# Kernel tuning notes

Measured on AMD Instinct MI355X. Metric: run time of the kernel, lower is better.

The kernel has to match this reference:

```python
import jax, jax.numpy as jnp
import numpy as np

H = 32          # num_attention_heads
KVH = 8         # num_key_value_heads
D = 2048        # hidden_size
HD = D // H     # attention_head_size = 64
REP = H // KVH  # queries per kv head = 4


def setup_inputs() -> dict:
    key = jax.random.key(0)
    ks = jax.random.split(key, 7)
    s = 0.02
    return {
        "hidden_states": jax.random.normal(ks[0], (2, 2048, D), dtype=jnp.float32),
        "Wq": jax.random.normal(ks[1], (D, D), dtype=jnp.float32) * s,
        "bq": jax.random.normal(ks[2], (D,), dtype=jnp.float32) * s,
        "Wk": jax.random.normal(ks[3], (D, KVH * HD), dtype=jnp.float32) * s,
        "bk": jax.random.normal(ks[4], (KVH * HD,), dtype=jnp.float32) * s,
        "Wv": jax.random.normal(ks[5], (D, KVH * HD), dtype=jnp.float32) * s,
        "bv": jax.random.normal(ks[6], (KVH * HD,), dtype=jnp.float32) * s,
    }


def _split_heads(x, n_heads):
    # [B, S, n_heads*HD] -> [B, n_heads, S, HD]
    b, s, _ = x.shape
    return x.reshape(b, s, n_heads, HD).transpose(0, 2, 1, 3)


def reference(hidden_states, Wq, bq, Wk, bk, Wv, bv):
    b, s, _ = hidden_states.shape
    q = _split_heads(hidden_states @ Wq + bq, H)          # [B,H,S,HD]
    k = _split_heads(hidden_states @ Wk + bk, KVH)        # [B,KVH,S,HD]
    v = _split_heads(hidden_states @ Wv + bv, KVH)
    # repeat KV heads to match query heads (q_idx // REP -> kv_idx)
    k = jnp.repeat(k, REP, axis=1)                         # [B,H,S,HD]
    v = jnp.repeat(v, REP, axis=1)
    scores = jnp.einsum("bhqd,bhkd->bhqk", q, k) / jnp.sqrt(jnp.float32(HD))
    probs = jax.nn.softmax(scores, axis=-1)
    ctx = jnp.einsum("bhqk,bhkd->bhqd", probs, v)          # [B,H,S,HD]
    ctx = ctx.transpose(0, 2, 1, 3).reshape(b, s, H * HD)
    return ctx
```

## Files before the change

### kernel.cpp

```cpp
#include <hip/hip_runtime.h>
#include <hip/hip_bf16.h>

#define NH 32
#define NKVH 8
#define DMODEL 2048
#define HDIM 64
#define NB 2
#define SEQ 2048
#define MROWS (NB*SEQ)
#define NQ 2048
#define NKV 512
#define NTOT 3072
#define NT (SEQ/64)

typedef __bf16 bf16x4 __attribute__((ext_vector_type(4)));
typedef __bf16 bf16x8 __attribute__((ext_vector_type(8)));
typedef float  f32x2  __attribute__((ext_vector_type(2)));
typedef float  f32x4  __attribute__((ext_vector_type(4)));
typedef float  f32x16 __attribute__((ext_vector_type(16)));
typedef unsigned u32x2 __attribute__((ext_vector_type(2)));
typedef unsigned u32x4 __attribute__((ext_vector_type(4)));

__device__ inline __bf16 f2bf(float f) {
    unsigned u = __builtin_bit_cast(unsigned, f);
    u += 0x7fff + ((u >> 16) & 1);
    unsigned short s = (unsigned short)(u >> 16);
    return __builtin_bit_cast(__bf16, s);
}

__device__ inline unsigned pack2bf(float a, float b) {
    unsigned ua = __builtin_bit_cast(unsigned, a);
    ua += 0x7fff + ((ua >> 16) & 1);
    unsigned ub = __builtin_bit_cast(unsigned, b);
    ub += 0x7fff + ((ub >> 16) & 1);
    return (ua >> 16) | (ub & 0xffff0000u);
}

__device__ inline void gload_lds16(const void* g, void* l) {
    __builtin_amdgcn_global_load_lds(
        (const __attribute__((address_space(1))) void*)g,
        (__attribute__((address_space(3))) void*)l, 16, 0, 0);
}

__device__ inline float max3f(float a, float b, float c) {
    float r;
    asm("v_max3_f32 %0, %1, %2, %3" : "=v"(r) : "v"(a), "v"(b), "v"(c));
    return r;
}

__device__ inline float cross_max32(float x) {
#if __has_builtin(__builtin_amdgcn_permlane32_swap)
    unsigned xu = __builtin_bit_cast(unsigned, x);
    u32x2 r = __builtin_amdgcn_permlane32_swap(xu, xu, false, false);
    return fmaxf(__builtin_bit_cast(float, r[0]), __builtin_bit_cast(float, r[1]));
#else
    return fmaxf(x, __shfl_xor(x, 32));
#endif
}

__global__ __launch_bounds__(256)
void cvt_hs(const float* __restrict__ Hs, __bf16* __restrict__ Ab)
{
    size_t idx = ((size_t)blockIdx.x * 256 + threadIdx.x) * 8;
    f32x4 a = *reinterpret_cast<const f32x4*>(Hs + idx);
    f32x4 b = *reinterpret_cast<const f32x4*>(Hs + idx + 4);
    u32x4 w;
    w[0] = pack2bf(a[0], a[1]); w[1] = pack2bf(a[2], a[3]);
    w[2] = pack2bf(b[0], b[1]); w[3] = pack2bf(b[2], b[3]);
    *reinterpret_cast<u32x4*>((char*)Ab + idx * 2) = w;
}

__global__ __launch_bounds__(256)
void transpose_w(const float* __restrict__ Wq,
                 const float* __restrict__ Wk,
                 const float* __restrict__ Wv,
                 __bf16* __restrict__ Wt)
{
    __shared__ __bf16 tile[64][72];
    int k0 = blockIdx.x * 64;
    int n0 = blockIdx.y * 64;
    const float* Wsrc; int ncols; int nbase;
    if (n0 < NQ)            { Wsrc = Wq; ncols = NQ;  nbase = n0; }
    else if (n0 < NQ + NKV) { Wsrc = Wk; ncols = NKV; nbase = n0 - NQ; }
    else                    { Wsrc = Wv; ncols = NKV; nbase = n0 - NQ - NKV; }
    int t = threadIdx.x;
    int kl = t >> 2;
    int nc = (t & 3) * 16;
    const float* src = Wsrc + (size_t)(k0 + kl) * ncols + nbase + nc;
    #pragma unroll
    for (int i = 0; i < 4; ++i) {
        f32x4 v = *reinterpret_cast<const f32x4*>(src + i * 4);
        #pragma unroll
        for (int e = 0; e < 4; ++e) tile[kl][nc + i * 4 + e] = f2bf(v[e]);
    }
    __syncthreads();
    int nl = t >> 2;
    int kc = (t & 3) * 16;
    bf16x8 o0, o1;
    #pragma unroll
    for (int i = 0; i < 8; ++i) o0[i] = tile[kc + i][nl];
    #pragma unroll
    for (int i = 0; i < 8; ++i) o1[i] = tile[kc + 8 + i][nl];
    __bf16* dst = Wt + (size_t)(n0 + nl) * DMODEL + k0 + kc;
    *reinterpret_cast<bf16x8*>(dst)     = o0;
    *reinterpret_cast<bf16x8*>(dst + 8) = o1;
}

#define BM 128
#define BN 128
#define BK 64

__global__ __launch_bounds__(256)
void qkv_gemm(const __bf16* __restrict__ Ab,
              const __bf16* __restrict__ Wt,
              const float* __restrict__ bq,
              const float* __restrict__ bk,
              const float* __restrict__ bv,
              __bf16* __restrict__ Qb,
              __bf16* __restrict__ Kb,
              __bf16* __restrict__ Vt)
{
    __shared__ char lds[32768];

    int bid = blockIdx.x;
    int xcd = bid & 7, r = bid >> 3;
    int rm = r / 12, rn = r % 12;
    int m0 = ((xcd >> 1) * 8 + rm) * BM;
    int n0 = ((xcd & 1) * 12 + rn) * BN;

    int t = threadIdx.x;
    int wave = t >> 6, lane = t & 63;
    int g = lane >> 4, lh = lane & 15;
    int wr = wave >> 1, wc = wave & 1;

    int srow = wave * 8 + (lane >> 3);
    int schunk = (lane & 7) ^ (lane >> 3);
    const char* Asrc = (const char*)Ab + (size_t)(m0 + srow) * 4096 + schunk * 16;
    const char* Bsrc = (const char*)Wt + (size_t)(n0 + srow) * 4096 + schunk * 16;
    int dstw = wave * 1024;

    f32x4 acc[4][4] = {};

    for (int k0 = 0; k0 < DMODEL * 2; k0 += BK * 2) {
        #pragma unroll
        for (int i = 0; i < 4; ++i)
            gload_lds16(Asrc + (size_t)i * 32 * 4096 + k0, lds + i * 4096 + dstw);
        #pragma unroll
        for (int i = 0; i < 4; ++i)
            gload_lds16(Bsrc + (size_t)i * 32 * 4096 + k0, lds + 16384 + i * 4096 + dstw);
        __syncthreads();
        #pragma unroll
        for (int kk = 0; kk < 2; ++kk) {
            bf16x8 af[4], bfr[4];
            #pragma unroll
            for (int mi = 0; mi < 4; ++mi) {
                int row = wr * 64 + mi * 16 + lh;
                int byte = row * 128 + (((kk * 4 + g) ^ (lh & 7)) << 4);
                af[mi] = *reinterpret_cast<const bf16x8*>(lds + byte);
            }
            #pragma unroll
            for (int ni = 0; ni < 4; ++ni) {
                int row = wc * 64 + ni * 16 + lh;
                int byte = row * 128 + (((kk * 4 + g) ^ (lh & 7)) << 4);
                bfr[ni] = *reinterpret_cast<const bf16x8*>(lds + 16384 + byte);
            }
            #pragma unroll
            for (int mi = 0; mi < 4; ++mi)
                #pragma unroll
                for (int ni = 0; ni < 4; ++ni)
                    acc[mi][ni] = __builtin_amdgcn_mfma_f32_16x16x32_bf16(af[mi], bfr[ni], acc[mi][ni], 0, 0, 0);
        }
        __syncthreads();
    }

    int mode = (n0 < NQ) ? 0 : (n0 < NQ + NKV ? 1 : 2);
    const float* bias = (mode == 0) ? bq : (mode == 1 ? bk : bv);
    int nsub = (mode == 0) ? 0 : (mode == 1 ? NQ : NQ + NKV);
    float scale = (mode == 0) ? 0.18033688011112042f : 1.0f;

    float biasv[4];
    #pragma unroll
    for (int ni = 0; ni < 4; ++ni)
        biasv[ni] = bias[n0 - nsub + wc * 64 + ni * 16 + lh];

    int gsw = ((g & 1) << 1) | (g >> 1);

    #pragma unroll
    for (int mi = 0; mi < 4; ++mi) {
        #pragma unroll
        for (int j = 0; j < 4; ++j) {
            int m = m0 + wr * 64 + mi * 16 + 4 * g + j;
            int bb = m >> 11, s = m & (SEQ - 1);
            #pragma unroll
            for (int ni = 0; ni < 4; ++ni) {
                int n = n0 + wc * 64 + ni * 16 + lh;
                __bf16 val = f2bf((acc[mi][ni][j] + biasv[ni]) * scale);
                if (mode == 0) {
                    int hh = n >> 6, d = n & 63;
                    Qb[(((size_t)bb * NH + hh) * SEQ + s) * HDIM + d] = val;
                } else if (mode == 1) {
                    int nk = n - NQ; int kv = nk >> 6, d = nk & 63;
                    Kb[(((size_t)bb * NKVH + kv) * SEQ + s) * HDIM + d] = val;
                } else {
                    int nv = n - NQ - NKV; int kv = nv >> 6, d = nv & 63;
                    int sv = (s & ~12) | (gsw << 2);
                    Vt[(((size_t)bb * NKVH + kv) * HDIM + d) * SEQ + sv] = val;
                }
            }
        }
    }
}

#define SUBSTEP(BUFB, SS) do { \
    bf16x8 kf0_ = *reinterpret_cast<const bf16x8*>(lds + (BUFB) + koff[(SS)*4 + 0]); \
    bf16x8 kf1_ = *reinterpret_cast<const bf16x8*>(lds + (BUFB) + koff[(SS)*4 + 1]); \
    bf16x8 kf2_ = *reinterpret_cast<const bf16x8*>(lds + (BUFB) + koff[(SS)*4 + 2]); \
    bf16x8 kf3_ = *reinterpret_cast<const bf16x8*>(lds + (BUFB) + koff[(SS)*4 + 3]); \
    f32x16 s_ = {}; \
    __builtin_amdgcn_s_setprio(1); \
    s_ = __builtin_amdgcn_mfma_f32_32x32x16_bf16(kf0_, qf[0], s_, 0, 0, 0); \
    s_ = __builtin_amdgcn_mfma_f32_32x32x16_bf16(kf1_, qf[1], s_, 0, 0, 0); \
    s_ = __builtin_amdgcn_mfma_f32_32x32x16_bf16(kf2_, qf[2], s_, 0, 0, 0); \
    s_ = __builtin_amdgcn_mfma_f32_32x32x16_bf16(kf3_, qf[3], s_, 0, 0, 0); \
    __builtin_amdgcn_s_setprio(0); \
    float n0_ = max3f(max3f(s_[0], s_[1], s_[2]),  max3f(s_[3], s_[4], s_[5]), \
                      max3f(s_[6], s_[7], s_[8])); \
    float n1_ = max3f(max3f(s_[9], s_[10], s_[11]), max3f(s_[12], s_[13], s_[14]), s_[15]); \
    float mt_ = cross_max32(fmaxf(n0_, n1_)); \
    if (!__all(mt_ <= m_run + 8.0f)) { \
        float mn_ = fmaxf(m_run, mt_); \
        float al_ = __builtin_amdgcn_exp2f(m_run - mn_); \
        m_run = mn_; msub = -mn_; \
        accO0 *= al_; accO1 *= al_; lsum *= al_; \
    } \
    _Pragma("unroll") \
    for (int r = 0; r < 16; ++r) s_[r] = __builtin_amdgcn_exp2f(s_[r] + msub); \
    bf16x8 pa_, pb_; \
    _Pragma("unroll") \
    for (int e = 0; e < 8; ++e) { pa_[e] = (__bf16)s_[e]; pb_[e] = (__bf16)s_[8 + e]; } \
    bf16x8 va0_ = *reinterpret_cast<const bf16x8*>(lds + (BUFB) + 8192 + koff[2 * (SS)]); \
    bf16x8 vb0_ = *reinterpret_cast<const bf16x8*>(lds + (BUFB) + 8192 + koff[2 * (SS) + 1]); \
    bf16x8 va1_ = *reinterpret_cast<const bf16x8*>(lds + (BUFB) + 8192 + koff[4 + 2 * (SS)]); \
    bf16x8 vb1_ = *reinterpret_cast<const bf16x8*>(lds + (BUFB) + 8192 + koff[4 + 2 * (SS) + 1]); \
    __builtin_amdgcn_s_setprio(1); \
    accO0 = __builtin_amdgcn_mfma_f32_32x32x16_bf16(va0_, pa_, accO0, 0, 0, 0); \
    lsum  = __builtin_amdgcn_mfma_f32_32x32x16_bf16(ones, pa_, lsum,  0, 0, 0); \
    accO0 = __builtin_amdgcn_mfma_f32_32x32x16_bf16(vb0_, pb_, accO0, 0, 0, 0); \
    lsum  = __builtin_amdgcn_mfma_f32_32x32x16_bf16(ones, pb_, lsum,  0, 0, 0); \
    accO1 = __builtin_amdgcn_mfma_f32_32x32x16_bf16(va1_, pa_, accO1, 0, 0, 0); \
    accO1 = __builtin_amdgcn_mfma_f32_32x32x16_bf16(vb1_, pb_, accO1, 0, 0, 0); \
    __builtin_amdgcn_s_setprio(0); \
} while (0)

#define TILE(BUFB, SBUFB, KT, STAGE, VM) do { \
    if (STAGE) { \
        gload_lds16(Kp + (size_t)((KT) + 2) * 8192 + kgoff, lds + (SBUFB) + kdst); \
        gload_lds16(Vp + (size_t)((KT) + 2) * 128  + vgoff, lds + (SBUFB) + vdst); \
    } \
    SUBSTEP(BUFB, 0); \
    SUBSTEP(BUFB, 1); \
    asm volatile("s_waitcnt vmcnt(" #VM ")" ::: "memory"); \
    __builtin_amdgcn_s_barrier(); \
} while (0)

__global__ __launch_bounds__(512, 4)
void attn(const __bf16* __restrict__ Qb,
          const __bf16* __restrict__ Kb,
          const __bf16* __restrict__ Vt,
          float* __restrict__ out)
{
    __shared__ char lds[65536];

    int qt = blockIdx.x;
    int bh = blockIdx.y;
    int b = bh >> 5, h = bh & 31;
    int kvh = h >> 2;
    int tid = threadIdx.x, wave = tid >> 6, lane = tid & 63;
    int ql = lane & 31, hi = lane >> 5;
    int q0 = qt * 256 + wave * 32;

    const __bf16* Qp = Qb + (size_t)(b * NH + h) * SEQ * HDIM;
    const char*   Kp = (const char*)(Kb + (size_t)(b * NKVH + kvh) * SEQ * HDIM);
    const char*   Vp = (const char*)(Vt + (size_t)(b * NKVH + kvh) * HDIM * SEQ);

    bf16x8 qf[4];
    #pragma unroll
    for (int f = 0; f < 4; ++f)
        qf[f] = *reinterpret_cast<const bf16x8*>(Qp + (size_t)(q0 + ql) * HDIM + f * 16 + hi * 8);

    u32x4 ou = { 0x3F803F80u, 0x3F803F80u, 0x3F803F80u, 0x3F803F80u };
    bf16x8 ones = __builtin_bit_cast(bf16x8, ou);

    int srow = tid >> 3;
    int schk = (tid & 7) ^ (srow & 7);
    int kgoff = srow * 128 + (schk << 4);
    size_t vgoff = (size_t)srow * (SEQ * 2) + (schk << 4);
    int kdst = tid * 16;
    int vdst = 8192 + tid * 16;

    int koff[8];
    #pragma unroll
    for (int kb = 0; kb < 2; ++kb)
        #pragma unroll
        for (int f = 0; f < 4; ++f)
            koff[kb * 4 + f] = (kb * 32 + ql) * 128 + ((f * 32 + hi * 16) ^ ((ql & 7) << 4));

    f32x16 accO0 = {}, accO1 = {}, lsum = {};
    float m_run = -1e30f, msub = 0.0f;

    gload_lds16(Kp + kgoff,        lds + kdst);
    gload_lds16(Vp + vgoff,        lds + vdst);
    gload_lds16(Kp + 8192 + kgoff, lds + 16384 + kdst);
    gload_lds16(Vp + 128  + vgoff, lds + 16384 + vdst);
    asm volatile("s_waitcnt vmcnt(2)" ::: "memory");
    __builtin_amdgcn_s_barrier();

    #pragma unroll 1
    for (int g4 = 0; g4 < 7; ++g4) {
        int kt = g4 * 4;
        TILE(0,     32768, kt + 0, true, 2);
        TILE(16384, 49152, kt + 1, true, 2);
        TILE(32768, 0,     kt + 2, true, 2);
        TILE(49152, 16384, kt + 3, true, 2);
    }
    TILE(0,     32768, 28, true,  2);
    TILE(16384, 49152, 29, true,  2);
    TILE(32768, 0,     30, false, 0);
    TILE(49152, 0,     31, false, 0);

    float inv = 1.0f / lsum[0];
    float* op = out + ((size_t)b * SEQ + q0 + ql) * DMODEL + h * HDIM;
    #pragma unroll
    for (int G = 0; G < 4; ++G) {
        f32x4 o0 = { accO0[4 * G + 0] * inv, accO0[4 * G + 1] * inv,
                     accO0[4 * G + 2] * inv, accO0[4 * G + 3] * inv };
        f32x4 o1 = { accO1[4 * G + 0] * inv, accO1[4 * G + 1] * inv,
                     accO1[4 * G + 2] * inv, accO1[4 * G + 3] * inv };
        *reinterpret_cast<f32x4*>(op + 8 * G + 4 * hi)      = o0;
        *reinterpret_cast<f32x4*>(op + 32 + 8 * G + 4 * hi) = o1;
    }
}

extern "C" void kernel_launch(void* const* d_in, const int* in_sizes, int n_in,
                              void* d_out, int out_size, void* d_ws, size_t ws_size,
                              hipStream_t stream)
{
    const float* hs = (const float*)d_in[0];
    const float* Wq = (const float*)d_in[1];
    const float* bq = (const float*)d_in[2];
    const float* Wk = (const float*)d_in[3];
    const float* bk = (const float*)d_in[4];
    const float* Wv = (const float*)d_in[5];
    const float* bv = (const float*)d_in[6];
    float* out = (float*)d_out;

    char* ws = (char*)d_ws;
    __bf16* Wt = (__bf16*)(ws);
    __bf16* Ab = (__bf16*)(ws + 12582912);
    __bf16* Qb = (__bf16*)(ws + 12582912 + 16777216);
    __bf16* Kb = (__bf16*)(ws + 12582912 + 2*16777216);
    __bf16* Vt = (__bf16*)(ws + 12582912 + 2*16777216 + 4194304);

    hipLaunchKernelGGL(cvt_hs,      dim3(4096),   dim3(256), 0, stream, hs, Ab);
    hipLaunchKernelGGL(transpose_w, dim3(32, 48), dim3(256), 0, stream, Wq, Wk, Wv, Wt);
    hipLaunchKernelGGL(qkv_gemm,    dim3(768),    dim3(256), 0, stream, Ab, Wt, bq, bk, bv, Qb, Kb, Vt);
    hipLaunchKernelGGL(attn,        dim3(8, 64),  dim3(512), 0, stream, Qb, Kb, Vt, out);
}
```

Before: 178.0 us.

## Enlarge QKV GEMM tiles to 256x192 with double-buffered LDS prefetch

The QKV projection GEMM moves from 128x128 tiles with 256 threads and a single LDS buffer to 256x192 tiles with 512 threads and two LDS buffers. The next K-slab is prefetched while MFMAs run on the current one, and s_setprio is raised around the MFMA bursts. The larger tiles cut global reloads per output and the double buffering hides load latency. In exchange, the grid shrinks to 256 blocks, which is about one per CU, and the kernel uses 112KB of LDS and more accumulator registers, so occupancy drops.

```diff
diff --git a/kernel.cpp b/kernel.cpp
--- a/kernel.cpp
+++ b/kernel.cpp
@@ -106,11 +106,20 @@
     *reinterpret_cast<bf16x8*>(dst + 8) = o1;
 }
 
-#define BM 128
-#define BN 128
-#define BK 64
-
-__global__ __launch_bounds__(256)
+#define GBM 256
+#define GBN 192
+#define GBUF 57344
+
+#define GSTAGE(NXT, KO) do { \
+    _Pragma("unroll") \
+    for (int i_ = 0; i_ < 4; ++i_) \
+        gload_lds16(Asrc + (size_t)i_ * 262144 + (KO), (NXT) + i_ * 8192 + dst); \
+    _Pragma("unroll") \
+    for (int i_ = 0; i_ < 3; ++i_) \
+        gload_lds16(Bsrc + (size_t)i_ * 262144 + (KO), (NXT) + 32768 + i_ * 8192 + dst); \
+} while (0)
+
+__global__ __launch_bounds__(512)
 void qkv_gemm(const __bf16* __restrict__ Ab,
               const __bf16* __restrict__ Wt,
               const float* __restrict__ bq,
@@ -120,81 +129,84 @@
               __bf16* __restrict__ Kb,
               __bf16* __restrict__ Vt)
 {
-    __shared__ char lds[32768];
+    __shared__ char lds[2 * GBUF];
 
     int bid = blockIdx.x;
-    int xcd = bid & 7, r = bid >> 3;
-    int rm = r / 12, rn = r % 12;
-    int m0 = ((xcd >> 1) * 8 + rm) * BM;
-    int n0 = ((xcd & 1) * 12 + rn) * BN;
-
-    int t = threadIdx.x;
-    int wave = t >> 6, lane = t & 63;
+    int xcd = bid & 7, idx = bid >> 3;
+    int mb = (xcd >> 1) * 4 + (idx >> 3);
+    int nb = (xcd & 1) * 8 + (idx & 7);
+    int m0 = mb * GBM, n0 = nb * GBN;
+
+    int tid = threadIdx.x, wave = tid >> 6, lane = tid & 63;
     int g = lane >> 4, lh = lane & 15;
-    int wr = wave >> 1, wc = wave & 1;
-
-    int srow = wave * 8 + (lane >> 3);
-    int schunk = (lane & 7) ^ (lane >> 3);
-    const char* Asrc = (const char*)Ab + (size_t)(m0 + srow) * 4096 + schunk * 16;
-    const char* Bsrc = (const char*)Wt + (size_t)(n0 + srow) * 4096 + schunk * 16;
-    int dstw = wave * 1024;
-
-    f32x4 acc[4][4] = {};
-
-    for (int k0 = 0; k0 < DMODEL * 2; k0 += BK * 2) {
-        #pragma unroll
-        for (int i = 0; i < 4; ++i)
-            gload_lds16(Asrc + (size_t)i * 32 * 4096 + k0, lds + i * 4096 + dstw);
-        #pragma unroll
-        for (int i = 0; i < 4; ++i)
-            gload_lds16(Bsrc + (size_t)i * 32 * 4096 + k0, lds + 16384 + i * 4096 + dstw);
-        __syncthreads();
-        #pragma unroll
-        for (int kk = 0; kk < 2; ++kk) {
-            bf16x8 af[4], bfr[4];
+    int wr = wave >> 2, wc = wave & 3;
+
+    int srow = tid >> 3;
+    int sb = ((tid & 7) ^ (srow & 7)) << 4;
+    const char* Asrc = (const char*)Ab + (size_t)(m0 + srow) * 4096 + sb;
+    const char* Bsrc = (const char*)Wt + (size_t)(n0 + srow) * 4096 + sb;
+    int dst = tid * 16;
+
+    f32x4 acc[8][3] = {};
+
+    GSTAGE(lds, 0);
+    __syncthreads();
+
+    #pragma unroll 1
+    for (int t = 0; t < NT; ++t) {
+        const char* cur = lds + (t & 1) * GBUF;
+        char* nxt = lds + ((t + 1) & 1) * GBUF;
+        if (t + 1 < NT) GSTAGE(nxt, (t + 1) * 128);
+        bf16x8 bfr[3][2];
+        #pragma unroll
+        for (int ni = 0; ni < 3; ++ni) {
+            int col = wc * 48 + ni * 16 + lh;
             #pragma unroll
-            for (int mi = 0; mi < 4; ++mi) {
-                int row = wr * 64 + mi * 16 + lh;
-                int byte = row * 128 + (((kk * 4 + g) ^ (lh & 7)) << 4);
-                af[mi] = *reinterpret_cast<const bf16x8*>(lds + byte);
+            for (int kk = 0; kk < 2; ++kk)
+                bfr[ni][kk] = *reinterpret_cast<const bf16x8*>(
+                    cur + 32768 + col * 128 + (((kk * 4 + g) ^ (lh & 7)) << 4));
+        }
+        #pragma unroll
+        for (int p = 0; p < 4; ++p) {
+            bf16x8 af[2][2];
+            #pragma unroll
+            for (int mi = 0; mi < 2; ++mi) {
+                int row = wr * 128 + p * 32 + mi * 16 + lh;
+                #pragma unroll
+                for (int kk = 0; kk < 2; ++kk)
+                    af[mi][kk] = *reinterpret_cast<const bf16x8*>(
+                        cur + row * 128 + (((kk * 4 + g) ^ (lh & 7)) << 4));
             }
+            __builtin_amdgcn_s_setprio(1);
             #pragma unroll
-            for (int ni = 0; ni < 4; ++ni) {
-                int row = wc * 64 + ni * 16 + lh;
-                int byte = row * 128 + (((kk * 4 + g) ^ (lh & 7)) << 4);
-                bfr[ni] = *reinterpret_cast<const bf16x8*>(lds + 16384 + byte);
-            }
-            #pragma unroll
-            for (int mi = 0; mi < 4; ++mi)
+            for (int kk = 0; kk < 2; ++kk)
                 #pragma unroll
-                for (int ni = 0; ni < 4; ++ni)
-                    acc[mi][ni] = __builtin_amdgcn_mfma_f32_16x16x32_bf16(af[mi], bfr[ni], acc[mi][ni], 0, 0, 0);
+                for (int mi = 0; mi < 2; ++mi)
+                    #pragma unroll
+                    for (int ni = 0; ni < 3; ++ni)
+                        acc[p * 2 + mi][ni] = __builtin_amdgcn_mfma_f32_16x16x32_bf16(
+                            af[mi][kk], bfr[ni][kk], acc[p * 2 + mi][ni], 0, 0, 0);
+            __builtin_amdgcn_s_setprio(0);
         }
         __syncthreads();
     }
 
-    int mode = (n0 < NQ) ? 0 : (n0 < NQ + NKV ? 1 : 2);
-    const float* bias = (mode == 0) ? bq : (mode == 1 ? bk : bv);
-    int nsub = (mode == 0) ? 0 : (mode == 1 ? NQ : NQ + NKV);
-    float scale = (mode == 0) ? 0.18033688011112042f : 1.0f;
-
-    float biasv[4];
-    #pragma unroll
-    for (int ni = 0; ni < 4; ++ni)
-        biasv[ni] = bias[n0 - nsub + wc * 64 + ni * 16 + lh];
-
     int gsw = ((g & 1) << 1) | (g >> 1);
-
-    #pragma unroll
-    for (int mi = 0; mi < 4; ++mi) {
-        #pragma unroll
-        for (int j = 0; j < 4; ++j) {
-            int m = m0 + wr * 64 + mi * 16 + 4 * g + j;
-            int bb = m >> 11, s = m & (SEQ - 1);
+    #pragma unroll
+    for (int ni = 0; ni < 3; ++ni) {
+        int n = n0 + wc * 48 + ni * 16 + lh;
+        int mode = (n < NQ) ? 0 : (n < NQ + NKV ? 1 : 2);
+        const float* bias = (mode == 0) ? bq : (mode == 1 ? bk : bv);
+        int nsub = (mode == 0) ? 0 : (mode == 1 ? NQ : NQ + NKV);
+        float scale = (mode == 0) ? 0.18033688011112042f : 1.0f;
+        float bval = bias[n - nsub];
+        #pragma unroll
+        for (int mi8 = 0; mi8 < 8; ++mi8) {
             #pragma unroll
-            for (int ni = 0; ni < 4; ++ni) {
-                int n = n0 + wc * 64 + ni * 16 + lh;
-                __bf16 val = f2bf((acc[mi][ni][j] + biasv[ni]) * scale);
+            for (int j = 0; j < 4; ++j) {
+                int m = m0 + wr * 128 + mi8 * 16 + 4 * g + j;
+                int bb = m >> 11, s = m & (SEQ - 1);
+                __bf16 val = f2bf((acc[mi8][ni][j] + bval) * scale);
                 if (mode == 0) {
                     int hh = n >> 6, d = n & 63;
                     Qb[(((size_t)bb * NH + hh) * SEQ + s) * HDIM + d] = val;
@@ -363,6 +375,6 @@
 
     hipLaunchKernelGGL(cvt_hs,      dim3(4096),   dim3(256), 0, stream, hs, Ab);
     hipLaunchKernelGGL(transpose_w, dim3(32, 48), dim3(256), 0, stream, Wq, Wk, Wv, Wt);
-    hipLaunchKernelGGL(qkv_gemm,    dim3(768),    dim3(256), 0, stream, Ab, Wt, bq, bk, bv, Qb, Kb, Vt);
+    hipLaunchKernelGGL(qkv_gemm,    dim3(256),    dim3(512), 0, stream, Ab, Wt, bq, bk, bv, Qb, Kb, Vt);
     hipLaunchKernelGGL(attn,        dim3(8, 64),  dim3(512), 0, stream, Qb, Kb, Vt, out);
 }
```

Result: faster. 160.8 us (median of 2 runs) (-9.7%).
